# Kernel optimization log

Hardware: AMD Instinct MI355X
Metric: run time of the kernel (lower is better)

## Reference

```python
import jax, jax.numpy as jnp
import numpy as np

WH, WW = 8, 8            # window_size
NUM_HEADS = 8
DIM = 256
CPB_HIDDEN = 512
N = WH * WW


def _make_coords_table():
    # [1, 2*WH-1, 2*WW-1, 2] log-spaced continuous relative coords (Swin-V2)
    h = np.arange(-(WH - 1), WH, dtype=np.float32)
    w = np.arange(-(WW - 1), WW, dtype=np.float32)
    gh, gw = np.meshgrid(h, w, indexing='ij')
    table = np.stack([gh, gw], axis=-1)[None]  # [1,2WH-1,2WW-1,2]
    table[..., 0] /= (WH - 1)
    table[..., 1] /= (WW - 1)
    table *= 8.0
    table = np.sign(table) * np.log2(np.abs(table) + 1.0) / np.log2(8.0)
    return jnp.asarray(table, dtype=jnp.float32)


def _make_rel_pos_index():
    ch = np.arange(WH)
    cw = np.arange(WW)
    coords = np.stack(np.meshgrid(ch, cw, indexing='ij'))   # [2,WH,WW]
    cf = coords.reshape(2, -1)                               # [2,N]
    rel = cf[:, :, None] - cf[:, None, :]                    # [2,N,N]
    rel = rel.transpose(1, 2, 0).astype(np.int32)            # [N,N,2]
    rel[..., 0] += WH - 1
    rel[..., 1] += WW - 1
    rel[..., 0] *= 2 * WW - 1
    return jnp.asarray(rel.sum(-1), dtype=jnp.int32)         # [N,N]


def setup_inputs() -> dict:
    key = jax.random.key(0)
    ks = jax.random.split(key, 8)
    B_ = 2048
    nW = 64
    x = jax.random.normal(ks[0], (B_, N, DIM), dtype=jnp.float32)
    mask = jnp.zeros((nW, N, N), dtype=jnp.float32)
    qkv_w = jax.random.normal(ks[1], (3 * DIM, DIM), dtype=jnp.float32) * 0.02
    q_bias = jnp.zeros((DIM,), dtype=jnp.float32)
    v_bias = jnp.zeros((DIM,), dtype=jnp.float32)
    logit_scale = jnp.log(10.0 * jnp.ones((NUM_HEADS, 1, 1), dtype=jnp.float32))
    cpb_w1 = jax.random.normal(ks[2], (CPB_HIDDEN, 2), dtype=jnp.float32) * 0.02
    cpb_b1 = jnp.zeros((CPB_HIDDEN,), dtype=jnp.float32)
    cpb_w2 = jax.random.normal(ks[3], (NUM_HEADS, CPB_HIDDEN), dtype=jnp.float32) * 0.02
    proj_w = jax.random.normal(ks[4], (DIM, DIM), dtype=jnp.float32) * 0.02
    proj_b = jnp.zeros((DIM,), dtype=jnp.float32)
    return {
        'x': x, 'mask': mask,
        'qkv_w': qkv_w, 'q_bias': q_bias, 'v_bias': v_bias,
        'logit_scale': logit_scale,
        'cpb_w1': cpb_w1, 'cpb_b1': cpb_b1, 'cpb_w2': cpb_w2,
        'proj_w': proj_w, 'proj_b': proj_b,
        'coords_table': _make_coords_table(),
        'rel_idx': _make_rel_pos_index(),
    }


def reference(x, mask, qkv_w, q_bias, v_bias, logit_scale,
              cpb_w1, cpb_b1, cpb_w2, proj_w, proj_b,
              coords_table, rel_idx):
    B_, n, C = x.shape
    H = NUM_HEADS
    hd = C // H

    # qkv with [q_bias, 0, v_bias]
    qkv_bias = jnp.concatenate([q_bias, jnp.zeros_like(v_bias), v_bias])
    qkv = x @ qkv_w.T + qkv_bias                         # [B,N,3C]
    qkv = qkv.reshape(B_, n, 3, H, hd).transpose(2, 0, 3, 1, 4)
    q, k, v = qkv[0], qkv[1], qkv[2]                     # [B,H,N,hd]

    # cosine attention: L2-normalized q,k (eps as in F.normalize)
    qn = q / jnp.maximum(jnp.linalg.norm(q, axis=-1, keepdims=True), 1e-12)
    kn = k / jnp.maximum(jnp.linalg.norm(k, axis=-1, keepdims=True), 1e-12)
    attn = jnp.einsum('bhnd,bhmd->bhnm', qn, kn)         # [B,H,N,N]

    max_log = jnp.log(jnp.asarray(1.0 / 0.01, dtype=x.dtype))
    scale = jnp.exp(jnp.minimum(logit_scale, max_log))   # [H,1,1]
    attn = attn * scale

    # MLP relative position bias: 2 -> 512 -> H, gather, 16*sigmoid
    hid = jax.nn.relu(coords_table @ cpb_w1.T + cpb_b1)  # [1,2WH-1,2WW-1,512]
    table = (hid @ cpb_w2.T).reshape(-1, H)              # [(2WH-1)(2WW-1), H]
    bias = table[rel_idx.reshape(-1)].reshape(n, n, H)
    bias = 16.0 * jax.nn.sigmoid(bias.transpose(2, 0, 1))  # [H,N,N]
    attn = attn + bias[None]

    nW = mask.shape[0]
    attn = attn.reshape(B_ // nW, nW, H, n, n) + mask[None, :, None]
    attn = attn.reshape(B_, H, n, n)
    attn = jax.nn.softmax(attn, axis=-1)

    out = jnp.einsum('bhnm,bhmd->bhnd', attn, v)         # [B,H,N,hd]
    out = out.transpose(0, 2, 1, 3).reshape(B_, n, C)
    return out @ proj_w.T + proj_b
```

## Files before the change

kernel.cpp:

```cpp
#include <hip/hip_runtime.h>
#include <hip/hip_bf16.h>

typedef unsigned short u16;
typedef unsigned int   u32;
typedef __attribute__((ext_vector_type(8))) short short8;
typedef __attribute__((ext_vector_type(4))) short short4v;
typedef __attribute__((ext_vector_type(4))) float f32x4;

__device__ __forceinline__ u16 f2bf(float f) {
  u32 u = __float_as_uint(f);
  u32 r = (u + 0x7fffu + ((u >> 16) & 1u)) >> 16;
  return (u16)r;
}

__global__ __launch_bounds__(256) void wcvt_kernel(
    const float* __restrict__ qkvw, const float* __restrict__ pw,
    u16* __restrict__ wq, u16* __restrict__ wp) {
  const int e = (blockIdx.x * 256 + threadIdx.x) * 4;
  if (e < 196608) {
    const float4 v = *(const float4*)(qkvw + e);
    short4v o; o[0]=(short)f2bf(v.x); o[1]=(short)f2bf(v.y);
    o[2]=(short)f2bf(v.z); o[3]=(short)f2bf(v.w);
    *(short4v*)(wq + e) = o;
  } else {
    const int e2 = e - 196608;
    const float4 v = *(const float4*)(pw + e2);
    short4v o; o[0]=(short)f2bf(v.x); o[1]=(short)f2bf(v.y);
    o[2]=(short)f2bf(v.z); o[3]=(short)f2bf(v.w);
    *(short4v*)(wp + e2) = o;
  }
}

__global__ __launch_bounds__(256) void cpb_kernel(
    const float* __restrict__ ct, const float* __restrict__ w1,
    const float* __restrict__ b1, const float* __restrict__ w2,
    float* __restrict__ table) {
  const int r = blockIdx.x;
  const int t = threadIdx.x;
  const int lane = t & 63, wave = t >> 6;
  const float c0 = ct[r * 2 + 0];
  const float c1 = ct[r * 2 + 1];
  float acc[8] = {0.f, 0.f, 0.f, 0.f, 0.f, 0.f, 0.f, 0.f};
  for (int j = t; j < 512; j += 256) {
    float hid = fmaxf(c0 * w1[j * 2] + c1 * w1[j * 2 + 1] + b1[j], 0.f);
#pragma unroll
    for (int hh = 0; hh < 8; ++hh) acc[hh] += hid * w2[hh * 512 + j];
  }
#pragma unroll
  for (int hh = 0; hh < 8; ++hh)
#pragma unroll
    for (int off = 1; off < 64; off <<= 1) acc[hh] += __shfl_xor(acc[hh], off);
  __shared__ float red[4][8];
  if (lane == 0)
#pragma unroll
    for (int hh = 0; hh < 8; ++hh) red[wave][hh] = acc[hh];
  __syncthreads();
  if (t < 8) table[r * 8 + t] = red[0][t] + red[1][t] + red[2][t] + red[3][t];
}

__global__ __launch_bounds__(256) void bm_kernel(
    const float* __restrict__ table, const int* __restrict__ rel,
    const float* __restrict__ mask, float* __restrict__ bmP) {
  const int g = blockIdx.x * 256 + threadIdx.x;
  const int w = g >> 13;
  const int h = (g >> 10) & 7;
  const int m = (g >> 4) & 63;
  const int l = g & 15;
  float4 o;
#pragma unroll
  for (int j = 0; j < 4; ++j) {
    const int c = j * 16 + l;
    const float t = table[rel[m * 64 + c] * 8 + h];
    o[j] = 16.f / (1.f + __expf(-t)) + mask[(size_t)w * 4096 + m * 64 + c];
  }
  *(float4*)(bmP + ((((size_t)w * 8 + h) * 64 + m) * 64 + l * 4)) = o;
}

__global__ __launch_bounds__(512, 2) void fused_kernel(
    const float* __restrict__ X,
    const float* __restrict__ bmP,
    const float* __restrict__ lsc,
    const u16*  __restrict__ Wqb,
    const float* __restrict__ qb, const float* __restrict__ vbias,
    const u16*  __restrict__ Wpb,
    const float* __restrict__ pb,
    float* __restrict__ out) {
  __shared__ __attribute__((aligned(16))) u16 sA[16896];
  __shared__ __attribute__((aligned(16))) u16 sW[8][6912];

  const int bw = blockIdx.x;
  const int w  = bw & 63;
  const int tid  = threadIdx.x;
  const int wave = tid >> 6, lane = tid & 63;
  const int l15 = lane & 15, l4 = lane >> 4;
  const int h = wave;

  {
    const int cq  = tid & 7;
    const int rlo = tid >> 3;
    const float* xrow = X + ((size_t)bw * 64 + rlo) * 256;
#pragma unroll
    for (int kf = 0; kf < 8; ++kf) {
      const float4 xv = *(const float4*)(xrow + kf * 32 + cq * 4);
      short4v t4; t4[0]=(short)f2bf(xv.x); t4[1]=(short)f2bf(xv.y);
      t4[2]=(short)f2bf(xv.z); t4[3]=(short)f2bf(xv.w);
      *(short4v*)&sA[kf * 2048 + rlo * 32 + cq * 4] = t4;
    }
  }
  __syncthreads();

  u16* vt   = &sW[wave][0];
  u16* pbuf = &sW[wave][2304];

  f32x4 oa[4][2];

  {
    const int rb[6] = {h * 32, h * 32 + 16, 256 + h * 32, 256 + h * 32 + 16,
                       512 + h * 32, 512 + h * 32 + 16};
    f32x4 acc[4][6];
#pragma unroll
    for (int mi = 0; mi < 4; ++mi)
#pragma unroll
      for (int nj = 0; nj < 6; ++nj) acc[mi][nj] = (f32x4){0.f, 0.f, 0.f, 0.f};

    short8 bf_cur[6];
#pragma unroll
    for (int nj = 0; nj < 6; ++nj)
      bf_cur[nj] = *(const short8*)(Wqb + (size_t)(rb[nj] + l15) * 256 + l4 * 8);

#pragma unroll
    for (int kf = 0; kf < 8; ++kf) {
      short8 af[4];
#pragma unroll
      for (int mi = 0; mi < 4; ++mi)
        af[mi] = *(const short8*)&sA[kf * 2048 + (mi * 16 + l15) * 32 + l4 * 8];
      short8 bf_nxt[6];
      if (kf < 7) {
#pragma unroll
        for (int nj = 0; nj < 6; ++nj)
          bf_nxt[nj] = *(const short8*)(Wqb + (size_t)(rb[nj] + l15) * 256 + (kf + 1) * 32 + l4 * 8);
      }
#pragma unroll
      for (int nj = 0; nj < 6; ++nj)
#pragma unroll
        for (int mi = 0; mi < 4; ++mi)
          acc[mi][nj] = __builtin_amdgcn_mfma_f32_16x16x32_bf16(af[mi], bf_cur[nj], acc[mi][nj], 0, 0, 0);
      if (kf < 7) {
#pragma unroll
        for (int nj = 0; nj < 6; ++nj) bf_cur[nj] = bf_nxt[nj];
      }
    }

    u16* qstage = pbuf;
    u16* kstage = pbuf + 2048;
    {
      const float qb0 = qb[h * 32 + l15];
      const float qb1 = qb[h * 32 + 16 + l15];
#pragma unroll
      for (int mi = 0; mi < 4; ++mi)
#pragma unroll
        for (int r = 0; r < 4; ++r) {
          const float v0 = acc[mi][0][r] + qb0;
          const float v1 = acc[mi][1][r] + qb1;
          float ss = v0 * v0 + v1 * v1;
          ss += __shfl_xor(ss, 1); ss += __shfl_xor(ss, 2);
          ss += __shfl_xor(ss, 4); ss += __shfl_xor(ss, 8);
          const float inv = 1.f / fmaxf(sqrtf(ss), 1e-12f);
          const int m = mi * 16 + l4 * 4 + r;
          qstage[m * 32 + l15]      = f2bf(v0 * inv);
          qstage[m * 32 + 16 + l15] = f2bf(v1 * inv);
        }
#pragma unroll
      for (int mi = 0; mi < 4; ++mi)
#pragma unroll
        for (int r = 0; r < 4; ++r) {
          const float v0 = acc[mi][2][r];
          const float v1 = acc[mi][3][r];
          float ss = v0 * v0 + v1 * v1;
          ss += __shfl_xor(ss, 1); ss += __shfl_xor(ss, 2);
          ss += __shfl_xor(ss, 4); ss += __shfl_xor(ss, 8);
          const float inv = 1.f / fmaxf(sqrtf(ss), 1e-12f);
          const int m = mi * 16 + l4 * 4 + r;
          kstage[m * 32 + l15]      = f2bf(v0 * inv);
          kstage[m * 32 + 16 + l15] = f2bf(v1 * inv);
        }
      const float vb0 = vbias[h * 32 + l15];
      const float vb1 = vbias[h * 32 + 16 + l15];
#pragma unroll
      for (int mi = 0; mi < 4; ++mi)
#pragma unroll
        for (int r = 0; r < 4; ++r) {
          const int m = mi * 16 + l4 * 4 + r;
          vt[l15 * 72 + m]        = f2bf(acc[mi][4][r] + vb0);
          vt[(16 + l15) * 72 + m] = f2bf(acc[mi][5][r] + vb1);
        }
    }

    const float* bmbase = bmP + (((size_t)(w * 8 + h)) * 64) * 64 + l15 * 4;
    float4 bmv[4][4];
#pragma unroll
    for (int i = 0; i < 4; ++i)
#pragma unroll
      for (int r = 0; r < 4; ++r) {
        const int m = i * 16 + l4 * 4 + r;
        bmv[i][r] = *(const float4*)(bmbase + (size_t)m * 64);
      }

    short8 aq[4], bk[4];
#pragma unroll
    for (int i = 0; i < 4; ++i)
      aq[i] = *(const short8*)&qstage[(i * 16 + l15) * 32 + l4 * 8];
#pragma unroll
    for (int j = 0; j < 4; ++j)
      bk[j] = *(const short8*)&kstage[(j * 16 + l15) * 32 + l4 * 8];

    f32x4 s[4][4];
    __builtin_amdgcn_s_setprio(1);
#pragma unroll
    for (int i = 0; i < 4; ++i)
#pragma unroll
      for (int j = 0; j < 4; ++j) {
        const f32x4 z = {0.f, 0.f, 0.f, 0.f};
        s[i][j] = __builtin_amdgcn_mfma_f32_16x16x32_bf16(aq[i], bk[j], z, 0, 0, 0);
      }
    __builtin_amdgcn_s_setprio(0);

    const float scale = __expf(fminf(lsc[h], 4.60517018598809136804f));
    u16* pW = pbuf;

#pragma unroll
    for (int i = 0; i < 4; ++i)
#pragma unroll
      for (int r = 0; r < 4; ++r) {
        const int m = i * 16 + l4 * 4 + r;
        float v0[4]; float mx = -3.0e38f;
#pragma unroll
        for (int j = 0; j < 4; ++j) {
          const float sv = s[i][j][r] * scale + bmv[i][r][j];
          v0[j] = sv; mx = fmaxf(mx, sv);
        }
        mx = fmaxf(mx, __shfl_xor(mx, 1)); mx = fmaxf(mx, __shfl_xor(mx, 2));
        mx = fmaxf(mx, __shfl_xor(mx, 4)); mx = fmaxf(mx, __shfl_xor(mx, 8));
        float sum = 0.f;
#pragma unroll
        for (int j = 0; j < 4; ++j) { v0[j] = __expf(v0[j] - mx); sum += v0[j]; }
        sum += __shfl_xor(sum, 1); sum += __shfl_xor(sum, 2);
        sum += __shfl_xor(sum, 4); sum += __shfl_xor(sum, 8);
        const float isum = 1.f / sum;
#pragma unroll
        for (int j = 0; j < 4; ++j)
          pW[m * 72 + j * 16 + l15] = f2bf(v0[j] * isum);
      }

#pragma unroll
    for (int i = 0; i < 4; ++i)
#pragma unroll
      for (int nb = 0; nb < 2; ++nb) oa[i][nb] = (f32x4){0.f, 0.f, 0.f, 0.f};
#pragma unroll
    for (int kb = 0; kb < 2; ++kb) {
      short8 pa[4];
#pragma unroll
      for (int i = 0; i < 4; ++i)
        pa[i] = *(const short8*)&pW[(i * 16 + l15) * 72 + kb * 32 + l4 * 8];
      __builtin_amdgcn_s_setprio(1);
#pragma unroll
      for (int nb = 0; nb < 2; ++nb) {
        const short8 vb8 = *(const short8*)&vt[(nb * 16 + l15) * 72 + kb * 32 + l4 * 8];
#pragma unroll
        for (int i = 0; i < 4; ++i)
          oa[i][nb] = __builtin_amdgcn_mfma_f32_16x16x32_bf16(pa[i], vb8, oa[i][nb], 0, 0, 0);
      }
      __builtin_amdgcn_s_setprio(0);
    }
  }

  __syncthreads();

#pragma unroll
  for (int i = 0; i < 4; ++i)
#pragma unroll
    for (int nb = 0; nb < 2; ++nb)
#pragma unroll
      for (int r = 0; r < 4; ++r) {
        const int m = i * 16 + l4 * 4 + r;
        sA[m * 264 + h * 32 + nb * 16 + l15] = f2bf(oa[i][nb][r]);
      }
  __syncthreads();

  {
    const int n0 = wave * 32;
    const u16* pbase = Wpb + (size_t)(n0 + l15) * 256 + l4 * 8;
    f32x4 pacc[4][2];
#pragma unroll
    for (int mi = 0; mi < 4; ++mi)
#pragma unroll
      for (int nj = 0; nj < 2; ++nj) pacc[mi][nj] = (f32x4){0.f, 0.f, 0.f, 0.f};

    short8 bfr_cur[2];
#pragma unroll
    for (int nj = 0; nj < 2; ++nj)
      bfr_cur[nj] = *(const short8*)(pbase + (size_t)(nj * 16) * 256);

#pragma unroll
    for (int ks = 0; ks < 8; ++ks) {
      const int k0 = ks * 32;
      short8 afr[4];
#pragma unroll
      for (int mi = 0; mi < 4; ++mi)
        afr[mi] = *(const short8*)&sA[(mi * 16 + l15) * 264 + k0 + l4 * 8];
      short8 bfr_nxt[2];
      if (ks < 7) {
#pragma unroll
        for (int nj = 0; nj < 2; ++nj)
          bfr_nxt[nj] = *(const short8*)(pbase + (size_t)(nj * 16) * 256 + k0 + 32);
      }
#pragma unroll
      for (int nj = 0; nj < 2; ++nj)
#pragma unroll
        for (int mi = 0; mi < 4; ++mi)
          pacc[mi][nj] = __builtin_amdgcn_mfma_f32_16x16x32_bf16(afr[mi], bfr_cur[nj], pacc[mi][nj], 0, 0, 0);
      if (ks < 7) {
#pragma unroll
        for (int nj = 0; nj < 2; ++nj) bfr_cur[nj] = bfr_nxt[nj];
      }
    }
    float* orow = out + (size_t)bw * 64 * 256;
#pragma unroll
    for (int mi = 0; mi < 4; ++mi)
#pragma unroll
      for (int nj = 0; nj < 2; ++nj) {
        const int n = n0 + nj * 16 + l15;
        const float bias = pb[n];
#pragma unroll
        for (int r = 0; r < 4; ++r) {
          const int m = mi * 16 + l4 * 4 + r;
          orow[(size_t)m * 256 + n] = pacc[mi][nj][r] + bias;
        }
      }
  }
}

extern "C" void kernel_launch(void* const* d_in, const int* in_sizes, int n_in,
                              void* d_out, int out_size, void* d_ws, size_t ws_size,
                              hipStream_t stream) {
  (void)in_sizes; (void)n_in; (void)out_size; (void)ws_size;
  const float* x    = (const float*)d_in[0];
  const float* mask = (const float*)d_in[1];
  const float* qkvw = (const float*)d_in[2];
  const float* qb   = (const float*)d_in[3];
  const float* vb   = (const float*)d_in[4];
  const float* lsc  = (const float*)d_in[5];
  const float* w1   = (const float*)d_in[6];
  const float* b1   = (const float*)d_in[7];
  const float* w2   = (const float*)d_in[8];
  const float* pw   = (const float*)d_in[9];
  const float* pb   = (const float*)d_in[10];
  const float* ct   = (const float*)d_in[11];
  const int* rel    = (const int*)d_in[12];
  float* out = (float*)d_out;

  char* ws = (char*)d_ws;
  float* table = (float*)(ws);
  u16* Wqb = (u16*)(ws + 262144);
  u16* Wpb = (u16*)(ws + 720896);
  float* bmP = (float*)(ws + (1 << 20));

  wcvt_kernel<<<256, 256, 0, stream>>>(qkvw, pw, Wqb, Wpb);
  cpb_kernel<<<225, 256, 0, stream>>>(ct, w1, b1, w2, table);
  bm_kernel<<<2048, 256, 0, stream>>>(table, rel, mask, bmP);
  fused_kernel<<<2048, 512, 0, stream>>>(x, bmP, lsc, Wqb, qb, vb,
                                         Wpb, pb, out);
}
```

Measured before the change: 472.9 us.

## Use packed bf16 converts, padded LDS layouts, exp2 softmax, deferred normalization

```diff
diff --git a/kernel.cpp b/kernel.cpp
--- a/kernel.cpp
+++ b/kernel.cpp
@@ -4,7 +4,6 @@
 typedef unsigned short u16;
 typedef unsigned int   u32;
 typedef __attribute__((ext_vector_type(8))) short short8;
-typedef __attribute__((ext_vector_type(4))) short short4v;
 typedef __attribute__((ext_vector_type(4))) float f32x4;
 
 __device__ __forceinline__ u16 f2bf(float f) {
@@ -12,6 +11,13 @@
   u32 r = (u + 0x7fffu + ((u >> 16) & 1u)) >> 16;
   return (u16)r;
 }
+__device__ __forceinline__ u32 cvtpk(float lo, float hi) {
+  u32 r;
+  asm("v_cvt_pk_bf16_f32 %0, %1, %2" : "=v"(r) : "v"(lo), "v"(hi));
+  return r;
+}
+
+#define LOG2E 1.4426950408889634f
 
 __global__ __launch_bounds__(256) void wcvt_kernel(
     const float* __restrict__ qkvw, const float* __restrict__ pw,
@@ -19,15 +25,17 @@
   const int e = (blockIdx.x * 256 + threadIdx.x) * 4;
   if (e < 196608) {
     const float4 v = *(const float4*)(qkvw + e);
-    short4v o; o[0]=(short)f2bf(v.x); o[1]=(short)f2bf(v.y);
-    o[2]=(short)f2bf(v.z); o[3]=(short)f2bf(v.w);
-    *(short4v*)(wq + e) = o;
+    u32 w0 = cvtpk(v.x, v.y), w1 = cvtpk(v.z, v.w);
+    *(uint2*)(wq + e) = make_uint2(w0, w1);
   } else {
     const int e2 = e - 196608;
-    const float4 v = *(const float4*)(pw + e2);
-    short4v o; o[0]=(short)f2bf(v.x); o[1]=(short)f2bf(v.y);
-    o[2]=(short)f2bf(v.z); o[3]=(short)f2bf(v.w);
-    *(short4v*)(wp + e2) = o;
+#pragma unroll
+    for (int q = 0; q < 4; ++q) {
+      const int idx = e2 + q;
+      const int n = idx >> 8, p = idx & 255;
+      const int c = (p & 0xE0) | ((p & 1) << 4) | ((p >> 1) & 15);
+      wp[idx] = f2bf(pw[n * 256 + c]);
+    }
   }
 }
 
@@ -71,7 +79,7 @@
   for (int j = 0; j < 4; ++j) {
     const int c = j * 16 + l;
     const float t = table[rel[m * 64 + c] * 8 + h];
-    o[j] = 16.f / (1.f + __expf(-t)) + mask[(size_t)w * 4096 + m * 64 + c];
+    o[j] = (16.f / (1.f + __expf(-t)) + mask[(size_t)w * 4096 + m * 64 + c]) * LOG2E;
   }
   *(float4*)(bmP + ((((size_t)w * 8 + h) * 64 + m) * 64 + l * 4)) = o;
 }
@@ -85,8 +93,8 @@
     const u16*  __restrict__ Wpb,
     const float* __restrict__ pb,
     float* __restrict__ out) {
-  __shared__ __attribute__((aligned(16))) u16 sA[16896];
-  __shared__ __attribute__((aligned(16))) u16 sW[8][6912];
+  __shared__ __attribute__((aligned(16))) u16 sA[20480];
+  __shared__ __attribute__((aligned(16))) u16 sW[8][7424];
 
   const int bw = blockIdx.x;
   const int w  = bw & 63;
@@ -102,57 +110,74 @@
 #pragma unroll
     for (int kf = 0; kf < 8; ++kf) {
       const float4 xv = *(const float4*)(xrow + kf * 32 + cq * 4);
-      short4v t4; t4[0]=(short)f2bf(xv.x); t4[1]=(short)f2bf(xv.y);
-      t4[2]=(short)f2bf(xv.z); t4[3]=(short)f2bf(xv.w);
-      *(short4v*)&sA[kf * 2048 + rlo * 32 + cq * 4] = t4;
+      *(uint2*)&sA[kf * 2560 + rlo * 40 + cq * 4] =
+          make_uint2(cvtpk(xv.x, xv.y), cvtpk(xv.z, xv.w));
     }
   }
   __syncthreads();
 
-  u16* vt   = &sW[wave][0];
-  u16* pbuf = &sW[wave][2304];
+  u16* vt = &sW[wave][0];
+  u16* pq = &sW[wave][2304];
+  u16* pk = &sW[wave][4864];
+  u16* pP = &sW[wave][2304];
 
   f32x4 oa[4][2];
+  float is_[4][4];
 
   {
     const int rb[6] = {h * 32, h * 32 + 16, 256 + h * 32, 256 + h * 32 + 16,
                        512 + h * 32, 512 + h * 32 + 16};
+    const u16* wb[6];
+#pragma unroll
+    for (int nj = 0; nj < 6; ++nj)
+      wb[nj] = Wqb + (size_t)(rb[nj] + l15) * 256 + l4 * 8;
+
     f32x4 acc[4][6];
 #pragma unroll
     for (int mi = 0; mi < 4; ++mi)
 #pragma unroll
       for (int nj = 0; nj < 6; ++nj) acc[mi][nj] = (f32x4){0.f, 0.f, 0.f, 0.f};
 
-    short8 bf_cur[6];
-#pragma unroll
-    for (int nj = 0; nj < 6; ++nj)
-      bf_cur[nj] = *(const short8*)(Wqb + (size_t)(rb[nj] + l15) * 256 + l4 * 8);
+    short8 bfA[6], bfB[6];
+#pragma unroll
+    for (int nj = 0; nj < 6; ++nj) bfA[nj] = *(const short8*)(wb[nj]);
+#pragma unroll
+    for (int nj = 0; nj < 6; ++nj) bfB[nj] = *(const short8*)(wb[nj] + 32);
 
 #pragma unroll
     for (int kf = 0; kf < 8; ++kf) {
       short8 af[4];
 #pragma unroll
       for (int mi = 0; mi < 4; ++mi)
-        af[mi] = *(const short8*)&sA[kf * 2048 + (mi * 16 + l15) * 32 + l4 * 8];
-      short8 bf_nxt[6];
-      if (kf < 7) {
+        af[mi] = *(const short8*)&sA[kf * 2560 + (mi * 16 + l15) * 40 + l4 * 8];
+      __builtin_amdgcn_s_setprio(1);
+      if ((kf & 1) == 0) {
 #pragma unroll
         for (int nj = 0; nj < 6; ++nj)
-          bf_nxt[nj] = *(const short8*)(Wqb + (size_t)(rb[nj] + l15) * 256 + (kf + 1) * 32 + l4 * 8);
-      }
-#pragma unroll
-      for (int nj = 0; nj < 6; ++nj)
-#pragma unroll
-        for (int mi = 0; mi < 4; ++mi)
-          acc[mi][nj] = __builtin_amdgcn_mfma_f32_16x16x32_bf16(af[mi], bf_cur[nj], acc[mi][nj], 0, 0, 0);
-      if (kf < 7) {
-#pragma unroll
-        for (int nj = 0; nj < 6; ++nj) bf_cur[nj] = bf_nxt[nj];
-      }
-    }
-
-    u16* qstage = pbuf;
-    u16* kstage = pbuf + 2048;
+#pragma unroll
+          for (int mi = 0; mi < 4; ++mi)
+            acc[mi][nj] = __builtin_amdgcn_mfma_f32_16x16x32_bf16(af[mi], bfA[nj], acc[mi][nj], 0, 0, 0);
+        __builtin_amdgcn_s_setprio(0);
+        if (kf < 6) {
+#pragma unroll
+          for (int nj = 0; nj < 6; ++nj)
+            bfA[nj] = *(const short8*)(wb[nj] + (kf + 2) * 32);
+        }
+      } else {
+#pragma unroll
+        for (int nj = 0; nj < 6; ++nj)
+#pragma unroll
+          for (int mi = 0; mi < 4; ++mi)
+            acc[mi][nj] = __builtin_amdgcn_mfma_f32_16x16x32_bf16(af[mi], bfB[nj], acc[mi][nj], 0, 0, 0);
+        __builtin_amdgcn_s_setprio(0);
+        if (kf < 6) {
+#pragma unroll
+          for (int nj = 0; nj < 6; ++nj)
+            bfB[nj] = *(const short8*)(wb[nj] + (kf + 2) * 32);
+        }
+      }
+    }
+
     {
       const float qb0 = qb[h * 32 + l15];
       const float qb1 = qb[h * 32 + 16 + l15];
@@ -165,10 +190,9 @@
           float ss = v0 * v0 + v1 * v1;
           ss += __shfl_xor(ss, 1); ss += __shfl_xor(ss, 2);
           ss += __shfl_xor(ss, 4); ss += __shfl_xor(ss, 8);
-          const float inv = 1.f / fmaxf(sqrtf(ss), 1e-12f);
+          const float inv = __frsqrt_rn(fmaxf(ss, 1e-24f));
           const int m = mi * 16 + l4 * 4 + r;
-          qstage[m * 32 + l15]      = f2bf(v0 * inv);
-          qstage[m * 32 + 16 + l15] = f2bf(v1 * inv);
+          *(u32*)&pq[m * 40 + l15 * 2] = cvtpk(v0 * inv, v1 * inv);
         }
 #pragma unroll
       for (int mi = 0; mi < 4; ++mi)
@@ -179,40 +203,40 @@
           float ss = v0 * v0 + v1 * v1;
           ss += __shfl_xor(ss, 1); ss += __shfl_xor(ss, 2);
           ss += __shfl_xor(ss, 4); ss += __shfl_xor(ss, 8);
-          const float inv = 1.f / fmaxf(sqrtf(ss), 1e-12f);
+          const float inv = __frsqrt_rn(fmaxf(ss, 1e-24f));
           const int m = mi * 16 + l4 * 4 + r;
-          kstage[m * 32 + l15]      = f2bf(v0 * inv);
-          kstage[m * 32 + 16 + l15] = f2bf(v1 * inv);
+          *(u32*)&pk[m * 40 + l15 * 2] = cvtpk(v0 * inv, v1 * inv);
         }
       const float vb0 = vbias[h * 32 + l15];
       const float vb1 = vbias[h * 32 + 16 + l15];
 #pragma unroll
-      for (int mi = 0; mi < 4; ++mi)
+      for (int nb = 0; nb < 2; ++nb) {
+        const float vb = nb ? vb1 : vb0;
+        u16* vrow = vt + (nb * 16 + l15) * 72 + l4 * 16;
 #pragma unroll
         for (int r = 0; r < 4; ++r) {
-          const int m = mi * 16 + l4 * 4 + r;
-          vt[l15 * 72 + m]        = f2bf(acc[mi][4][r] + vb0);
-          vt[(16 + l15) * 72 + m] = f2bf(acc[mi][5][r] + vb1);
-        }
-    }
-
-    const float* bmbase = bmP + (((size_t)(w * 8 + h)) * 64) * 64 + l15 * 4;
+          const u32 w0 = cvtpk(acc[0][4 + nb][r] + vb, acc[1][4 + nb][r] + vb);
+          const u32 w1 = cvtpk(acc[2][4 + nb][r] + vb, acc[3][4 + nb][r] + vb);
+          *(uint2*)&vrow[r * 4] = make_uint2(w0, w1);
+        }
+      }
+    }
+
+    const float* bmbase = bmP + ((size_t)(w * 8 + h)) * 4096 + l15 * 4;
     float4 bmv[4][4];
 #pragma unroll
     for (int i = 0; i < 4; ++i)
 #pragma unroll
-      for (int r = 0; r < 4; ++r) {
-        const int m = i * 16 + l4 * 4 + r;
-        bmv[i][r] = *(const float4*)(bmbase + (size_t)m * 64);
-      }
+      for (int r = 0; r < 4; ++r)
+        bmv[i][r] = *(const float4*)(bmbase + (size_t)(i * 16 + l4 * 4 + r) * 64);
 
     short8 aq[4], bk[4];
 #pragma unroll
-    for (int i = 0; i < 4; ++i)
-      aq[i] = *(const short8*)&qstage[(i * 16 + l15) * 32 + l4 * 8];
-#pragma unroll
     for (int j = 0; j < 4; ++j)
-      bk[j] = *(const short8*)&kstage[(j * 16 + l15) * 32 + l4 * 8];
+      bk[j] = *(const short8*)&pk[(j * 16 + l15) * 40 + l4 * 8];
+#pragma unroll
+    for (int i = 0; i < 4; ++i)
+      aq[i] = *(const short8*)&pq[(i * 16 + l15) * 40 + l4 * 8];
 
     f32x4 s[4][4];
     __builtin_amdgcn_s_setprio(1);
@@ -225,8 +249,7 @@
       }
     __builtin_amdgcn_s_setprio(0);
 
-    const float scale = __expf(fminf(lsc[h], 4.60517018598809136804f));
-    u16* pW = pbuf;
+    const float sc2 = __expf(fminf(lsc[h], 4.60517018598809136804f)) * LOG2E;
 
 #pragma unroll
     for (int i = 0; i < 4; ++i)
@@ -236,20 +259,19 @@
         float v0[4]; float mx = -3.0e38f;
 #pragma unroll
         for (int j = 0; j < 4; ++j) {
-          const float sv = s[i][j][r] * scale + bmv[i][r][j];
+          const float sv = s[i][j][r] * sc2 + bmv[i][r][j];
           v0[j] = sv; mx = fmaxf(mx, sv);
         }
         mx = fmaxf(mx, __shfl_xor(mx, 1)); mx = fmaxf(mx, __shfl_xor(mx, 2));
         mx = fmaxf(mx, __shfl_xor(mx, 4)); mx = fmaxf(mx, __shfl_xor(mx, 8));
         float sum = 0.f;
 #pragma unroll
-        for (int j = 0; j < 4; ++j) { v0[j] = __expf(v0[j] - mx); sum += v0[j]; }
+        for (int j = 0; j < 4; ++j) { v0[j] = exp2f(v0[j] - mx); sum += v0[j]; }
         sum += __shfl_xor(sum, 1); sum += __shfl_xor(sum, 2);
         sum += __shfl_xor(sum, 4); sum += __shfl_xor(sum, 8);
-        const float isum = 1.f / sum;
-#pragma unroll
-        for (int j = 0; j < 4; ++j)
-          pW[m * 72 + j * 16 + l15] = f2bf(v0[j] * isum);
+        is_[i][r] = 1.f / sum;
+        *(uint2*)&pP[m * 72 + l15 * 4] =
+            make_uint2(cvtpk(v0[0], v0[1]), cvtpk(v0[2], v0[3]));
       }
 
 #pragma unroll
@@ -261,7 +283,7 @@
       short8 pa[4];
 #pragma unroll
       for (int i = 0; i < 4; ++i)
-        pa[i] = *(const short8*)&pW[(i * 16 + l15) * 72 + kb * 32 + l4 * 8];
+        pa[i] = *(const short8*)&pP[(i * 16 + l15) * 72 + kb * 32 + l4 * 8];
       __builtin_amdgcn_s_setprio(1);
 #pragma unroll
       for (int nb = 0; nb < 2; ++nb) {
@@ -279,12 +301,12 @@
 #pragma unroll
   for (int i = 0; i < 4; ++i)
 #pragma unroll
-    for (int nb = 0; nb < 2; ++nb)
-#pragma unroll
-      for (int r = 0; r < 4; ++r) {
-        const int m = i * 16 + l4 * 4 + r;
-        sA[m * 264 + h * 32 + nb * 16 + l15] = f2bf(oa[i][nb][r]);
-      }
+    for (int r = 0; r < 4; ++r) {
+      const int m = i * 16 + l4 * 4 + r;
+      const float is = is_[i][r];
+      *(u32*)&sA[m * 264 + h * 32 + l15 * 2] =
+          cvtpk(oa[i][0][r] * is, oa[i][1][r] * is);
+    }
   __syncthreads();
 
   {
```

Result: faster. 433.4 us (-8.4%).
